# Optimization experiments

Hardware: AMD Instinct MI355X
Metric: run time of the kernel (lower is better)

## Reference

```python
import jax, jax.numpy as jnp
import numpy as np

B, T, E = 2, 512, 1024        # batch, max_tokens, embedding dim
S, A = 2048, 30               # num_spans, max_arg_span


def setup_inputs() -> dict:
    key = jax.random.key(0)
    k1, k2, k3, k4 = jax.random.split(key, 4)
    x = jax.random.normal(k1, (B, T, E), dtype=jnp.float32)
    W = jax.random.normal(k2, (E, 1), dtype=jnp.float32) * (1.0 / np.sqrt(E))
    b = jnp.zeros((1,), dtype=jnp.float32)
    start = jax.random.randint(k3, (S,), 0, T, dtype=jnp.int32)
    width = jax.random.randint(k4, (S,), 1, A + 1, dtype=jnp.int32)
    end = jnp.minimum(start + width - 1, T - 1).astype(jnp.int32)
    return {"x": x, "W": W, "b": b, "start": start, "end": end}


def reference(x, W, b, start, end):
    # span_indices: clamp start+offset to last token, shape [S, A]
    span_idx = jnp.minimum(jnp.arange(A)[None, :] + start[:, None], T - 1)
    # gather span token embeddings: [B, S, A, E]
    span_emb = x[:, span_idx, :]
    # tiny per-token head score: Dense(1, relu) -> [B, T, 1]
    head_scores = jax.nn.relu(x @ W + b)
    # validity mask over span positions (log-mask), [S, A]
    span_width = end - start + 1
    valid = jnp.arange(A)[None, :] < span_width[:, None]
    log_mask = jnp.where(valid, 0.0, -jnp.inf)
    # gather scores per span position, add log-mask: [B, S, A, 1]
    span_head = head_scores[:, span_idx, :] + log_mask[None, :, :, None]
    # softmax over span-position axis (axis=2)
    attn = jax.nn.softmax(span_head, axis=2)
    # weighted-sum pooling over span positions -> [B, S, E]
    return jnp.sum(span_emb * attn, axis=2)
```

## Files before the change

kernel.cpp:

```cpp
#include <hip/hip_runtime.h>
#include <math.h>

#define TT 512
#define EE 1024
#define AA 30
#define CH 32
#define NC (TT / CH)

typedef float f32x4 __attribute__((ext_vector_type(4)));

static __device__ __forceinline__ float dot4(f32x4 p, f32x4 q) {
    return p.x * q.x + p.y * q.y + p.z * q.z + p.w * q.w;
}

__global__ __launch_bounds__(256) void score_kernel(const float* __restrict__ x,
                                                    const float* __restrict__ W,
                                                    const float* __restrict__ bias,
                                                    float* __restrict__ es, int BT) {
    int row  = blockIdx.x * 4 + (threadIdx.x >> 6);
    int lane = threadIdx.x & 63;
    if (row >= BT) return;
    const f32x4* xr = reinterpret_cast<const f32x4*>(x + (size_t)row * EE);
    const f32x4* wr = reinterpret_cast<const f32x4*>(W);
    float acc = 0.f;
    #pragma unroll
    for (int k = 0; k < 4; ++k) {
        int i = lane + 64 * k;
        acc += dot4(xr[i], wr[i]);
    }
    #pragma unroll
    for (int off = 32; off; off >>= 1) acc += __shfl_xor(acc, off, 64);
    if (lane == 0) es[row] = __expf(fmaxf(acc + bias[0], 0.0f));
}

__global__ __launch_bounds__(256) void prefix_kernel(const float* __restrict__ x,
                                                     const float* __restrict__ es,
                                                     float* __restrict__ Pp,
                                                     float* __restrict__ C) {
    int blk = blockIdx.x;
    int b = blk / NC, tc = blk - b * NC;
    int t0 = tc * CH;
    size_t rowoff = ((size_t)b * TT + t0) * (EE / 4);
    const f32x4* xb = reinterpret_cast<const f32x4*>(x) + rowoff + threadIdx.x;
    f32x4*       pp = reinterpret_cast<f32x4*>(Pp)      + rowoff + threadIdx.x;
    const float* e  = es + b * TT + t0;
    f32x4 acc = (f32x4)(0.f);
    #pragma unroll 8
    for (int i = 0; i < CH; ++i) {
        acc += e[i] * xb[(size_t)i * (EE / 4)];
        pp[(size_t)i * (EE / 4)] = acc;
    }
    reinterpret_cast<f32x4*>(C)[((size_t)b * NC + tc) * (EE / 4) + threadIdx.x] = acc;
}

template <int SWZ>
__global__ __launch_bounds__(256) void combine_kernel(const float* __restrict__ Pp,
                                                      const float* __restrict__ C,
                                                      const float* __restrict__ es,
                                                      const int* __restrict__ start,
                                                      const int* __restrict__ end,
                                                      float* __restrict__ out,
                                                      int S, int G) {
    int bid  = blockIdx.x;
    int wv   = threadIdx.x >> 6;
    int lane = threadIdx.x & 63;
    int b, s, g;
    if (SWZ) {
        int xcd = bid & 7;
        b = xcd >> 2;
        int local = ((bid >> 3) << 2) | (xcd & 3);
        s = local * 4 + wv;
        g = b * S + s;
    } else {
        g = bid * 4 + wv;
        if (g >= G) return;
        b = g / S;
        s = g - b * S;
    }

    int st = start[s];
    int nA = min(end[s] - st + 1, AA);
    int en = st + nA - 1;

    float ev = (lane < nA) ? es[b * TT + st + lane] : 0.f;
    #pragma unroll
    for (int off = 32; off; off >>= 1) ev += __shfl_xor(ev, off, 64);
    float inv = 1.0f / ev;

    const f32x4* base = reinterpret_cast<const f32x4*>(Pp + (size_t)b * TT * EE) + lane;
    const f32x4* pe = base + (size_t)en * (EE / 4);
    f32x4 n0 = pe[0], n1 = pe[64], n2 = pe[128], n3 = pe[192];
    if (st & (CH - 1)) {
        const f32x4* ps = base + (size_t)(st - 1) * (EE / 4);
        n0 -= ps[0]; n1 -= ps[64]; n2 -= ps[128]; n3 -= ps[192];
    }
    int cs = st / CH, ce = en / CH;
    if (ce > cs) {
        const f32x4* pc = reinterpret_cast<const f32x4*>(C + ((size_t)b * NC + cs) * EE) + lane;
        n0 += pc[0]; n1 += pc[64]; n2 += pc[128]; n3 += pc[192];
    }

    f32x4* op = reinterpret_cast<f32x4*>(out + (size_t)g * EE) + lane;
    __builtin_nontemporal_store(n0 * inv, op);
    __builtin_nontemporal_store(n1 * inv, op + 64);
    __builtin_nontemporal_store(n2 * inv, op + 128);
    __builtin_nontemporal_store(n3 * inv, op + 192);
}

template <int SWZ>
__global__ __launch_bounds__(256) void fused_span_kernel(const float* __restrict__ x,
                                                         const float* __restrict__ W,
                                                         const float* __restrict__ bias,
                                                         const int* __restrict__ start,
                                                         const int* __restrict__ end,
                                                         float* __restrict__ out,
                                                         int S, int G) {
    int bid  = blockIdx.x;
    int wv   = threadIdx.x >> 6;
    int lane = threadIdx.x & 63;
    int b, s, g;
    if (SWZ) {
        int xcd = bid & 7;
        b = xcd >> 2;
        int local = ((bid >> 3) << 2) | (xcd & 3);
        s = local * 4 + wv;
        g = b * S + s;
    } else {
        g = bid * 4 + wv;
        if (g >= G) return;
        b = g / S;
        s = g - b * S;
    }
    int st = start[s];
    int nA = min(end[s] - st + 1, AA);
    const f32x4* xb = reinterpret_cast<const f32x4*>(x + ((size_t)b * TT + st) * EE) + lane;
    const f32x4* wp = reinterpret_cast<const f32x4*>(W) + lane;
    f32x4 w0 = wp[0], w1 = wp[64], w2 = wp[128], w3 = wp[192];
    f32x4 a0 = (f32x4)(0.f), a1 = (f32x4)(0.f), a2 = (f32x4)(0.f), a3 = (f32x4)(0.f);
    float sum = 0.f, bsc = bias[0];
    for (int a = 0; a < nA; ++a) {
        const f32x4* r0 = xb + (size_t)a * (EE / 4);
        f32x4 v0 = r0[0], v1 = r0[64], v2 = r0[128], v3 = r0[192];
        float d0 = dot4(v0, w0) + dot4(v1, w1) + dot4(v2, w2) + dot4(v3, w3);
        #pragma unroll
        for (int off = 32; off; off >>= 1) d0 += __shfl_xor(d0, off, 64);
        float p0 = __expf(fmaxf(d0 + bsc, 0.f));
        sum += p0;
        a0 += p0 * v0; a1 += p0 * v1; a2 += p0 * v2; a3 += p0 * v3;
    }
    float inv = 1.0f / sum;
    f32x4* op = reinterpret_cast<f32x4*>(out + (size_t)g * EE) + lane;
    __builtin_nontemporal_store(a0 * inv, op);
    __builtin_nontemporal_store(a1 * inv, op + 64);
    __builtin_nontemporal_store(a2 * inv, op + 128);
    __builtin_nontemporal_store(a3 * inv, op + 192);
}

extern "C" void kernel_launch(void* const* d_in, const int* in_sizes, int n_in,
                              void* d_out, int out_size, void* d_ws, size_t ws_size,
                              hipStream_t stream) {
    const float* x     = (const float*)d_in[0];
    const float* W     = (const float*)d_in[1];
    const float* bias  = (const float*)d_in[2];
    const int*   start = (const int*)d_in[3];
    const int*   end   = (const int*)d_in[4];
    float*       out   = (float*)d_out;

    const int BT = in_sizes[0] / EE;
    const int S  = in_sizes[3];
    const int B  = BT / TT;
    const int G  = B * S;

    float* es = (float*)d_ws;
    float* Pp = (float*)((char*)d_ws + 8192);
    float* C  = (float*)((char*)d_ws + 8192 + (size_t)BT * EE * 4);
    size_t need = 8192 + (size_t)BT * EE * 4 + (size_t)B * NC * EE * 4;

    bool fast = (ws_size >= need) && (B * TT == BT) && (BT % 4 == 0);
    if (fast) {
        score_kernel<<<BT / 4, 256, 0, stream>>>(x, W, bias, es, BT);
        prefix_kernel<<<B * NC, 256, 0, stream>>>(x, es, Pp, C);
        if (B == 2 && S == 2048)
            combine_kernel<1><<<G / 4, 256, 0, stream>>>(Pp, C, es, start, end, out, S, G);
        else
            combine_kernel<0><<<(G + 3) / 4, 256, 0, stream>>>(Pp, C, es, start, end, out, S, G);
    } else {
        if (B == 2 && S == 2048)
            fused_span_kernel<1><<<G / 4, 256, 0, stream>>>(x, W, bias, start, end, out, S, G);
        else
            fused_span_kernel<0><<<(G + 3) / 4, 256, 0, stream>>>(x, W, bias, start, end, out, S, G);
    }
}
```

Before: 20.74 us.

## Fuse score and prefix kernels, shrink chunk to 16, branchless combine

Merges the per-token score kernel into the chunked prefix-sum kernel, so each block computes its chunk's exp-scores into shared memory before the scan. This removes one launch and doubles the number of prefix blocks by halving the chunk size. Because a span of up to 30 tokens can now cross two chunk boundaries, the combine kernel adds a second chunk total. It loads all four operands unconditionally and blends them with 0/1 factors instead of branching. It also drops the XCD-aware block swizzle, which may hurt L2 locality on the combine pass.

```diff
diff --git a/kernel.cpp b/kernel.cpp
--- a/kernel.cpp
+++ b/kernel.cpp
@@ -4,7 +4,7 @@
 #define TT 512
 #define EE 1024
 #define AA 30
-#define CH 32
+#define CH 16
 #define NC (TT / CH)
 
 typedef float f32x4 __attribute__((ext_vector_type(4)));
@@ -13,47 +13,50 @@
     return p.x * q.x + p.y * q.y + p.z * q.z + p.w * q.w;
 }
 
-__global__ __launch_bounds__(256) void score_kernel(const float* __restrict__ x,
-                                                    const float* __restrict__ W,
-                                                    const float* __restrict__ bias,
-                                                    float* __restrict__ es, int BT) {
-    int row  = blockIdx.x * 4 + (threadIdx.x >> 6);
-    int lane = threadIdx.x & 63;
-    if (row >= BT) return;
-    const f32x4* xr = reinterpret_cast<const f32x4*>(x + (size_t)row * EE);
-    const f32x4* wr = reinterpret_cast<const f32x4*>(W);
-    float acc = 0.f;
-    #pragma unroll
-    for (int k = 0; k < 4; ++k) {
-        int i = lane + 64 * k;
-        acc += dot4(xr[i], wr[i]);
-    }
-    #pragma unroll
-    for (int off = 32; off; off >>= 1) acc += __shfl_xor(acc, off, 64);
-    if (lane == 0) es[row] = __expf(fmaxf(acc + bias[0], 0.0f));
-}
-
-__global__ __launch_bounds__(256) void prefix_kernel(const float* __restrict__ x,
-                                                     const float* __restrict__ es,
-                                                     float* __restrict__ Pp,
-                                                     float* __restrict__ C) {
+__global__ __launch_bounds__(256) void score_prefix_kernel(const float* __restrict__ x,
+                                                           const float* __restrict__ W,
+                                                           const float* __restrict__ bias,
+                                                           float* __restrict__ es,
+                                                           float* __restrict__ Pp,
+                                                           float* __restrict__ C) {
     int blk = blockIdx.x;
     int b = blk / NC, tc = blk - b * NC;
     int t0 = tc * CH;
-    size_t rowoff = ((size_t)b * TT + t0) * (EE / 4);
-    const f32x4* xb = reinterpret_cast<const f32x4*>(x) + rowoff + threadIdx.x;
-    f32x4*       pp = reinterpret_cast<f32x4*>(Pp)      + rowoff + threadIdx.x;
-    const float* e  = es + b * TT + t0;
+
+    __shared__ float es_s[CH];
+    int wv   = threadIdx.x >> 6;
+    int lane = threadIdx.x & 63;
+
+    const f32x4* wp = reinterpret_cast<const f32x4*>(W) + lane;
+    f32x4 w0 = wp[0], w1 = wp[64], w2 = wp[128], w3 = wp[192];
+    float bsc = bias[0];
+    #pragma unroll
+    for (int k = 0; k < CH / 4; ++k) {
+        int idx = wv + 4 * k;
+        const f32x4* xr = reinterpret_cast<const f32x4*>(x + ((size_t)b * TT + t0 + idx) * EE) + lane;
+        float d = dot4(xr[0], w0) + dot4(xr[64], w1) + dot4(xr[128], w2) + dot4(xr[192], w3);
+        #pragma unroll
+        for (int off = 32; off; off >>= 1) d += __shfl_xor(d, off, 64);
+        if (lane == 0) {
+            float e = __expf(fmaxf(d + bsc, 0.0f));
+            es_s[idx] = e;
+            es[b * TT + t0 + idx] = e;
+        }
+    }
+    __syncthreads();
+
+    size_t rowoff = ((size_t)b * TT + t0) * (EE / 4) + threadIdx.x;
+    const f32x4* xb = reinterpret_cast<const f32x4*>(x) + rowoff;
+    f32x4*       pp = reinterpret_cast<f32x4*>(Pp)      + rowoff;
     f32x4 acc = (f32x4)(0.f);
-    #pragma unroll 8
+    #pragma unroll
     for (int i = 0; i < CH; ++i) {
-        acc += e[i] * xb[(size_t)i * (EE / 4)];
+        acc += es_s[i] * xb[(size_t)i * (EE / 4)];
         pp[(size_t)i * (EE / 4)] = acc;
     }
     reinterpret_cast<f32x4*>(C)[((size_t)b * NC + tc) * (EE / 4) + threadIdx.x] = acc;
 }
 
-template <int SWZ>
 __global__ __launch_bounds__(256) void combine_kernel(const float* __restrict__ Pp,
                                                       const float* __restrict__ C,
                                                       const float* __restrict__ es,
@@ -61,22 +64,10 @@
                                                       const int* __restrict__ end,
                                                       float* __restrict__ out,
                                                       int S, int G) {
-    int bid  = blockIdx.x;
-    int wv   = threadIdx.x >> 6;
+    int g = blockIdx.x * 4 + (threadIdx.x >> 6);
+    if (g >= G) return;
     int lane = threadIdx.x & 63;
-    int b, s, g;
-    if (SWZ) {
-        int xcd = bid & 7;
-        b = xcd >> 2;
-        int local = ((bid >> 3) << 2) | (xcd & 3);
-        s = local * 4 + wv;
-        g = b * S + s;
-    } else {
-        g = bid * 4 + wv;
-        if (g >= G) return;
-        b = g / S;
-        s = g - b * S;
-    }
+    int b = g / S, s = g - b * S;
 
     int st = start[s];
     int nA = min(end[s] - st + 1, AA);
@@ -87,53 +78,51 @@
     for (int off = 32; off; off >>= 1) ev += __shfl_xor(ev, off, 64);
     float inv = 1.0f / ev;
 
-    const f32x4* base = reinterpret_cast<const f32x4*>(Pp + (size_t)b * TT * EE) + lane;
-    const f32x4* pe = base + (size_t)en * (EE / 4);
-    f32x4 n0 = pe[0], n1 = pe[64], n2 = pe[128], n3 = pe[192];
-    if (st & (CH - 1)) {
-        const f32x4* ps = base + (size_t)(st - 1) * (EE / 4);
-        n0 -= ps[0]; n1 -= ps[64]; n2 -= ps[128]; n3 -= ps[192];
-    }
-    int cs = st / CH, ce = en / CH;
-    if (ce > cs) {
-        const f32x4* pc = reinterpret_cast<const f32x4*>(C + ((size_t)b * NC + cs) * EE) + lane;
-        n0 += pc[0]; n1 += pc[64]; n2 += pc[128]; n3 += pc[192];
-    }
+    int cs = st >> 4, ce = en >> 4;
+    float fs = (st & (CH - 1)) ? 1.f : 0.f;
+    float f1 = (ce > cs)       ? 1.f : 0.f;
+    float f2 = (ce > cs + 1)   ? 1.f : 0.f;
+    int stm = st > 0 ? st - 1 : 0;
+    int c2  = cs + 1 < NC ? cs + 1 : NC - 1;
+
+    const f32x4* pb = reinterpret_cast<const f32x4*>(Pp) + (size_t)b * TT * (EE / 4) + lane;
+    const f32x4* cb = reinterpret_cast<const f32x4*>(C)  + (size_t)b * NC * (EE / 4) + lane;
+    const f32x4* pe = pb + (size_t)en  * (EE / 4);
+    const f32x4* ps = pb + (size_t)stm * (EE / 4);
+    const f32x4* g1 = cb + (size_t)cs  * (EE / 4);
+    const f32x4* g2 = cb + (size_t)c2  * (EE / 4);
+
+    f32x4 e0 = pe[0], e1 = pe[64], e2 = pe[128], e3 = pe[192];
+    f32x4 s0 = ps[0], s1 = ps[64], s2 = ps[128], s3 = ps[192];
+    f32x4 a0 = g1[0], a1 = g1[64], a2 = g1[128], a3 = g1[192];
+    f32x4 b0 = g2[0], b1 = g2[64], b2 = g2[128], b3 = g2[192];
+
+    f32x4 n0 = (e0 + f1 * a0 + f2 * b0 - fs * s0) * inv;
+    f32x4 n1 = (e1 + f1 * a1 + f2 * b1 - fs * s1) * inv;
+    f32x4 n2 = (e2 + f1 * a2 + f2 * b2 - fs * s2) * inv;
+    f32x4 n3 = (e3 + f1 * a3 + f2 * b3 - fs * s3) * inv;
 
     f32x4* op = reinterpret_cast<f32x4*>(out + (size_t)g * EE) + lane;
-    __builtin_nontemporal_store(n0 * inv, op);
-    __builtin_nontemporal_store(n1 * inv, op + 64);
-    __builtin_nontemporal_store(n2 * inv, op + 128);
-    __builtin_nontemporal_store(n3 * inv, op + 192);
+    __builtin_nontemporal_store(n0, op);
+    __builtin_nontemporal_store(n1, op + 64);
+    __builtin_nontemporal_store(n2, op + 128);
+    __builtin_nontemporal_store(n3, op + 192);
 }
 
-template <int SWZ>
 __global__ __launch_bounds__(256) void fused_span_kernel(const float* __restrict__ x,
                                                          const float* __restrict__ W,
                                                          const float* __restrict__ bias,
                                                          const int* __restrict__ start,
                                                          const int* __restrict__ end,
                                                          float* __restrict__ out,
-                                                         int S, int G) {
-    int bid  = blockIdx.x;
-    int wv   = threadIdx.x >> 6;
+                                                         int S, int G, int T) {
+    int g = blockIdx.x * 4 + (threadIdx.x >> 6);
+    if (g >= G) return;
     int lane = threadIdx.x & 63;
-    int b, s, g;
-    if (SWZ) {
-        int xcd = bid & 7;
-        b = xcd >> 2;
-        int local = ((bid >> 3) << 2) | (xcd & 3);
-        s = local * 4 + wv;
-        g = b * S + s;
-    } else {
-        g = bid * 4 + wv;
-        if (g >= G) return;
-        b = g / S;
-        s = g - b * S;
-    }
+    int b = g / S, s = g - b * S;
     int st = start[s];
     int nA = min(end[s] - st + 1, AA);
-    const f32x4* xb = reinterpret_cast<const f32x4*>(x + ((size_t)b * TT + st) * EE) + lane;
+    const f32x4* xb = reinterpret_cast<const f32x4*>(x + ((size_t)b * T + st) * EE) + lane;
     const f32x4* wp = reinterpret_cast<const f32x4*>(W) + lane;
     f32x4 w0 = wp[0], w1 = wp[64], w2 = wp[128], w3 = wp[192];
     f32x4 a0 = (f32x4)(0.f), a1 = (f32x4)(0.f), a2 = (f32x4)(0.f), a3 = (f32x4)(0.f);
@@ -176,18 +165,11 @@
     float* C  = (float*)((char*)d_ws + 8192 + (size_t)BT * EE * 4);
     size_t need = 8192 + (size_t)BT * EE * 4 + (size_t)B * NC * EE * 4;
 
-    bool fast = (ws_size >= need) && (B * TT == BT) && (BT % 4 == 0);
+    bool fast = (ws_size >= need) && (B * TT == BT) && (B >= 1);
     if (fast) {
-        score_kernel<<<BT / 4, 256, 0, stream>>>(x, W, bias, es, BT);
-        prefix_kernel<<<B * NC, 256, 0, stream>>>(x, es, Pp, C);
-        if (B == 2 && S == 2048)
-            combine_kernel<1><<<G / 4, 256, 0, stream>>>(Pp, C, es, start, end, out, S, G);
-        else
-            combine_kernel<0><<<(G + 3) / 4, 256, 0, stream>>>(Pp, C, es, start, end, out, S, G);
+        score_prefix_kernel<<<B * NC, 256, 0, stream>>>(x, W, bias, es, Pp, C);
+        combine_kernel<<<(G + 3) / 4, 256, 0, stream>>>(Pp, C, es, start, end, out, S, G);
     } else {
-        if (B == 2 && S == 2048)
-            fused_span_kernel<1><<<G / 4, 256, 0, stream>>>(x, W, bias, start, end, out, S, G);
-        else
-            fused_span_kernel<0><<<(G + 3) / 4, 256, 0, stream>>>(x, W, bias, start, end, out, S, G);
+        fused_span_kernel<<<(G + 3) / 4, 256, 0, stream>>>(x, W, bias, start, end, out, S, G, BT / B);
     }
 }
```

After: 20.72 us. About the same (-0.1%).
